# Performance work log

Measured on AMD Instinct MI355X. Metric: run time of the kernel, lower is better.

The kernel has to match this reference:

```python
import jax, jax.numpy as jnp
import numpy as np

N, D, R, E = 50000, 256, 4, 800000
LN_EPS = 1e-5
NEG_INF = -1e30  # finite stand-in for -inf so softmax stays grad-safe


def _layernorm(x, g, b):
    m = x.mean(axis=-1, keepdims=True)
    v = x.var(axis=-1, keepdims=True)
    return (x - m) / jnp.sqrt(v + LN_EPS) * g + b


def setup_inputs() -> dict:
    key = jax.random.key(0)
    ks = jax.random.split(key, 8)
    s = 1.0 / np.sqrt(D).astype(np.float32)
    return {
        'rows': jax.random.randint(ks[0], (R, E), 0, N),
        'cols': jax.random.randint(ks[1], (R, E), 0, N),
        'vals': jax.random.uniform(ks[2], (R, E), jnp.float32),
        'node_emb': jax.random.normal(ks[3], (N, D), jnp.float32) * s,
        'pre_W': jax.random.normal(ks[4], (D, D), jnp.float32) * s,
        'pre_b': jnp.zeros((D,), jnp.float32),
        'ln1_g': jnp.ones((D,), jnp.float32),
        'ln1_b': jnp.zeros((D,), jnp.float32),
        'rel_W': jax.random.normal(ks[5], (R, D, D), jnp.float32) * s,
        'attn_vec': jax.random.normal(ks[6], (D,), jnp.float32) * s,
        'self_W': jax.random.normal(ks[7], (D, D), jnp.float32) * s,
        'self_b': jnp.zeros((D,), jnp.float32),
        'bias': jnp.zeros((D,), jnp.float32),
        'ln2_g': jnp.ones((D,), jnp.float32),
        'ln2_b': jnp.zeros((D,), jnp.float32),
    }


def reference(rows, cols, vals, node_emb, pre_W, pre_b, ln1_g, ln1_b, rel_W,
              attn_vec, self_W, self_b, bias, ln2_g, ln2_b):
    # active_indices = arange(N), so x_all is the full embedding table
    x_all = node_emb
    # pre_encoder: Linear -> LayerNorm -> GELU (exact erf, torch default)
    x = jax.nn.gelu(_layernorm(x_all @ pre_W + pre_b, ln1_g, ln1_b), approximate=False)
    # per-relation: relation linear then SpMM (adj_t @ x_rel) via gather + segment_sum
    msgs = []
    for i in range(R):
        x_rel = x @ rel_W[i]                              # [N, D]
        contrib = vals[i][:, None] * x_rel[cols[i]]       # [E, D]
        msgs.append(jax.ops.segment_sum(contrib, rows[i], num_segments=N))
    stacked = jnp.stack(msgs, axis=1)                     # [N, R, D]
    # semantic attention over relations
    scores = jnp.einsum('nrd,d->nr', stacked, attn_vec)   # [N, R]
    mask = jnp.any(stacked != 0, axis=2)                  # [N, R]
    attn = jax.nn.softmax(jnp.where(mask, scores, NEG_INF), axis=1)
    attn = attn * mask                                    # == nan_to_num(softmax(-inf rows))
    out = jnp.einsum('nrd,nr->nd', stacked, attn) + bias + (x @ self_W + self_b)
    out = jax.nn.gelu(out, approximate=False)
    # active_indices = arange(N): scatter into global index space is identity
    final = _layernorm(out, ln2_g, ln2_b)
    return final, attn, x_all
```

## Files before the change

kernel.cpp:

```cpp
#include <hip/hip_runtime.h>
#include <hip/hip_fp16.h>
#include <math.h>


typedef __attribute__((ext_vector_type(8))) short bf16x8;
typedef __attribute__((ext_vector_type(4))) float f32x4;
typedef __attribute__((ext_vector_type(4))) unsigned u32x4;
typedef unsigned long long u64;

__device__ __forceinline__ float gelu_exact(float v) {
    return 0.5f * v * (1.0f + erff(v * 0.70710678118654752f));
}
__device__ __forceinline__ unsigned short f2bf(float f) {
    unsigned u = __float_as_uint(f);
    return (unsigned short)((u + 0x7fffu + ((u >> 16) & 1u)) >> 16);
}
__device__ __forceinline__ unsigned pack2(float a, float b) {
    return (unsigned)f2bf(a) | ((unsigned)f2bf(b) << 16);
}
__device__ __forceinline__ unsigned short f2h(float f) {
    return __half_as_ushort(__float2half(f));
}
__device__ __forceinline__ __half2 u2h2(unsigned u) {
    union { unsigned u; __half2 h; } c; c.u = u; return c.h;
}
__device__ __forceinline__ void gload16(const void* g, void* l) {
    __builtin_amdgcn_global_load_lds(
        (const __attribute__((address_space(1))) void*)g,
        (__attribute__((address_space(3))) void*)l, 16, 0, 0);
}

__global__ __launch_bounds__(256)
void conv_emb(const float* __restrict__ ne, unsigned short* __restrict__ emb,
              float* __restrict__ outX, int total4)
{
    const int stride = gridDim.x * blockDim.x;
    for (int i = blockIdx.x * blockDim.x + threadIdx.x; i < total4; i += stride) {
        const float4 v = reinterpret_cast<const float4*>(ne)[i];
        reinterpret_cast<float4*>(outX)[i] = v;
        ushort4 h;
        h.x = f2bf(v.x); h.y = f2bf(v.y); h.z = f2bf(v.z); h.w = f2bf(v.w);
        reinterpret_cast<ushort4*>(emb)[i] = h;
    }
}

__global__ __launch_bounds__(256)
void build_bt(const float* __restrict__ relW, const float* __restrict__ selfW,
              const float* __restrict__ preW, unsigned short* __restrict__ BTm,
              unsigned short* __restrict__ BTp)
{
    const int idx = blockIdx.x * 256 + threadIdx.x;
    if (idx < 1280 * 256) {
        const int k = idx >> 8, n = idx & 255;
        const float v = (k < 1024)
            ? relW[(size_t)(k >> 8) * 65536 + (size_t)(k & 255) * 256 + n]
            : selfW[(size_t)(k - 1024) * 256 + n];
        BTm[(size_t)n * 1280 + k] = f2bf(v);
    } else {
        const int i2 = idx - 1280 * 256;
        if (i2 < 256 * 256) {
            const int k = i2 >> 8, n = i2 & 255;
            BTp[(size_t)n * 256 + k] = f2bf(preW[(size_t)k * 256 + n]);
        }
    }
}

template<int MODE>
__global__ __launch_bounds__(512)
void gemm_mfma(const unsigned short* __restrict__ a0,
               const unsigned short* __restrict__ a1,
               const unsigned short* __restrict__ a2,
               const unsigned short* __restrict__ a3,
               const unsigned short* __restrict__ a4,
               const unsigned short* __restrict__ BT,
               const float* __restrict__ bias0, const float* __restrict__ bias1,
               const float* __restrict__ lng, const float* __restrict__ lnb,
               float* __restrict__ Cout, unsigned short* __restrict__ XOut,
               unsigned short* __restrict__ XH, int M)
{
    constexpr int K    = MODE ? 1280 : 256;
    constexpr int NSEG = MODE ? 5 : 1;

    __shared__ __align__(16) unsigned char smA[128 * 128];
    __shared__ __align__(16) unsigned char smB[256 * 128];
    __shared__ float redS[4][128];
    __shared__ float redQ[4][128];

    const int tid = threadIdx.x;
    const int w   = tid >> 6;
    const int l   = tid & 63;
    const int wm  = w >> 2, wn = w & 3;
    const int brow = blockIdx.x * 128;

    const int srow = l >> 3;
    const int sgA  = (l & 7) ^ srow;

    f32x4 acc[4][4];
#pragma unroll
    for (int mb = 0; mb < 4; ++mb)
#pragma unroll
        for (int nb = 0; nb < 4; ++nb)
            acc[mb][nb] = f32x4{0.f, 0.f, 0.f, 0.f};

    for (int seg = 0; seg < NSEG; ++seg) {
        const unsigned short* Abase =
            (MODE == 0) ? a0
                        : (seg == 0 ? a0 : seg == 1 ? a1 : seg == 2 ? a2
                                         : seg == 3 ? a3 : a4);
#pragma unroll
        for (int kk = 0; kk < 4; ++kk) {
            __syncthreads();
#pragma unroll
            for (int c = 0; c < 2; ++c) {
                const int r0 = (w * 2 + c) * 8;
                int gm = brow + r0 + srow;
                gm = min(gm, M - 1);
                gload16(Abase + ((size_t)gm << 8) + kk * 64 + sgA * 8,
                        smA + (w * 2 + c) * 1024);
            }
#pragma unroll
            for (int c = 0; c < 4; ++c) {
                const int bn = (w * 4 + c) * 8 + srow;
                gload16(BT + (size_t)bn * K + (seg * 4 + kk) * 64 + sgA * 8,
                        smB + (w * 4 + c) * 1024);
            }
            __syncthreads();

#pragma unroll
            for (int ks = 0; ks < 2; ++ks) {
                bf16x8 af[4], bf[4];
#pragma unroll
                for (int mb = 0; mb < 4; ++mb) {
                    const int row = wm * 64 + mb * 16 + (l & 15);
                    const int g   = (ks * 4 + (l >> 4)) ^ (row & 7);
                    af[mb] = *reinterpret_cast<const bf16x8*>(smA + row * 128 + g * 16);
                }
#pragma unroll
                for (int nb = 0; nb < 4; ++nb) {
                    const int row = wn * 64 + nb * 16 + (l & 15);
                    const int g   = (ks * 4 + (l >> 4)) ^ (row & 7);
                    bf[nb] = *reinterpret_cast<const bf16x8*>(smB + row * 128 + g * 16);
                }
#pragma unroll
                for (int mb = 0; mb < 4; ++mb)
#pragma unroll
                    for (int nb = 0; nb < 4; ++nb)
                        acc[mb][nb] = __builtin_amdgcn_mfma_f32_16x16x32_bf16(
                            af[mb], bf[nb], acc[mb][nb], 0, 0, 0);
            }
        }
    }

    float bb[4], gw[4], bw[4];
#pragma unroll
    for (int nb = 0; nb < 4; ++nb) {
        const int n = wn * 64 + nb * 16 + (l & 15);
        bb[nb] = bias0[n] + (MODE == 1 ? bias1[n] : 0.0f);
        gw[nb] = lng[n];
        bw[nb] = lnb[n];
    }
#pragma unroll
    for (int mb = 0; mb < 4; ++mb)
#pragma unroll
        for (int nb = 0; nb < 4; ++nb)
#pragma unroll
            for (int rg = 0; rg < 4; ++rg) {
                float v = acc[mb][nb][rg] + bb[nb];
                if (MODE == 1) v = gelu_exact(v);
                acc[mb][nb][rg] = v;
            }
#pragma unroll
    for (int mb = 0; mb < 4; ++mb)
#pragma unroll
        for (int rg = 0; rg < 4; ++rg) {
            float s = 0.f, q = 0.f;
#pragma unroll
            for (int nb = 0; nb < 4; ++nb) {
                const float v = acc[mb][nb][rg];
                s += v; q += v * v;
            }
#pragma unroll
            for (int off = 1; off < 16; off <<= 1) {
                s += __shfl_xor(s, off, 64);
                q += __shfl_xor(q, off, 64);
            }
            if ((l & 15) == 0) {
                const int row = wm * 64 + mb * 16 + (l >> 4) * 4 + rg;
                redS[wn][row] = s;
                redQ[wn][row] = q;
            }
        }
    __syncthreads();
    if (tid < 128) {
        const float s = redS[0][tid] + redS[1][tid] + redS[2][tid] + redS[3][tid];
        const float q = redQ[0][tid] + redQ[1][tid] + redQ[2][tid] + redQ[3][tid];
        const float mean = s * (1.0f / 256.0f);
        const float var  = q * (1.0f / 256.0f) - mean * mean;
        redS[0][tid] = mean;
        redQ[0][tid] = rsqrtf(var + 1e-5f);
    }
    __syncthreads();
#pragma unroll
    for (int mb = 0; mb < 4; ++mb)
#pragma unroll
        for (int rg = 0; rg < 4; ++rg) {
            const int row = wm * 64 + mb * 16 + (l >> 4) * 4 + rg;
            if (brow + row >= M) continue;
            const float mu = redS[0][row];
            const float rs = redQ[0][row];
#pragma unroll
            for (int nb = 0; nb < 4; ++nb) {
                const int n = wn * 64 + nb * 16 + (l & 15);
                const float v = (acc[mb][nb][rg] - mu) * rs * gw[nb] + bw[nb];
                if (MODE == 0) {
                    const float gv = gelu_exact(v);
                    XOut[((size_t)(brow + row) << 8) + n] = f2bf(gv);
                    XH[((size_t)(brow + row) << 8) + n]   = f2h(gv);
                } else {
                    Cout[((size_t)(brow + row) << 8) + n] = v;
                }
            }
        }
}

__global__ __launch_bounds__(256)
void wtilde_kernel(const float* __restrict__ relW, const float* __restrict__ av,
                   float* __restrict__ wt)
{
    __shared__ float avs[256];
    const int r = blockIdx.x, tid = threadIdx.x;
    avs[tid] = av[tid];
    __syncthreads();
    const float* W = relW + (size_t)r * 65536 + (size_t)tid * 256;
    float s = 0.f;
    for (int j = 0; j < 256; j += 4) {
        const float4 w4 = *reinterpret_cast<const float4*>(W + j);
        s += w4.x * avs[j] + w4.y * avs[j + 1] + w4.z * avs[j + 2] + w4.w * avs[j + 3];
    }
    wt[r * 256 + tid] = s;
}

__global__ __launch_bounds__(256)
void y_kernel(const unsigned short* __restrict__ XB, const float* __restrict__ wt,
              float* __restrict__ y, int Nn)
{
    const int n = blockIdx.x * 4 + (threadIdx.x >> 6);
    if (n >= Nn) return;
    const int l = threadIdx.x & 63;
    const uint2 d = *reinterpret_cast<const uint2*>(XB + ((size_t)n << 8) + l * 4);
    float xv[4];
    xv[0] = __uint_as_float(d.x << 16);
    xv[1] = __uint_as_float(d.x & 0xffff0000u);
    xv[2] = __uint_as_float(d.y << 16);
    xv[3] = __uint_as_float(d.y & 0xffff0000u);
    float s[4];
#pragma unroll
    for (int r = 0; r < 4; ++r) {
        const float4 w4 = *reinterpret_cast<const float4*>(wt + r * 256 + l * 4);
        s[r] = xv[0] * w4.x + xv[1] * w4.y + xv[2] * w4.z + xv[3] * w4.w;
#pragma unroll
        for (int off = 32; off; off >>= 1) s[r] += __shfl_xor(s[r], off, 64);
    }
    if (l == 0)
        *reinterpret_cast<float4*>(y + (size_t)n * 4) = make_float4(s[0], s[1], s[2], s[3]);
}

__global__ __launch_bounds__(256)
void hist_bin(const int* __restrict__ rows, int* __restrict__ cnt_t,
              int RE, int E, int Nn, int chunk, int NBIN)
{
    __shared__ int lh[800];
    const int blk = blockIdx.x;
    for (int i = threadIdx.x; i < NBIN; i += 256) lh[i] = 0;
    __syncthreads();
    const int e0 = blk * chunk;
    const int e1 = min(e0 + chunk, RE);
    for (int e = e0 + threadIdx.x; e < e1; e += 256) {
        const int r   = e / E;
        const int wid = r * Nn + rows[e];
        atomicAdd(&lh[wid >> 8], 1);
    }
    __syncthreads();
    for (int i = threadIdx.x; i < NBIN; i += 256)
        cnt_t[i * gridDim.x + blk] = lh[i];
}

__global__ __launch_bounds__(256)
void scan_blocks(const int* __restrict__ counts, int* __restrict__ offs,
                 int* __restrict__ bsums, int n)
{
    __shared__ int sh[256];
    const int t = threadIdx.x;
    const int base = blockIdx.x * 1024 + t * 4;
    int v[4], s = 0;
#pragma unroll
    for (int j = 0; j < 4; ++j) {
        v[j] = (base + j < n) ? counts[base + j] : 0;
        s += v[j];
    }
    sh[t] = s;
    __syncthreads();
    for (int off = 1; off < 256; off <<= 1) {
        const int x = (t >= off) ? sh[t - off] : 0;
        __syncthreads();
        sh[t] += x;
        __syncthreads();
    }
    int run = sh[t] - s;
    if (t == 255) bsums[blockIdx.x] = sh[255];
#pragma unroll
    for (int j = 0; j < 4; ++j) {
        if (base + j < n) offs[base + j] = run;
        run += v[j];
    }
}

__global__ __launch_bounds__(256)
void scan_bsums(int* __restrict__ bsums, int nblk)
{
    __shared__ int sh[256];
    const int t = threadIdx.x;
    const int v = (t < nblk) ? bsums[t] : 0;
    sh[t] = v;
    __syncthreads();
    for (int off = 1; off < 256; off <<= 1) {
        const int x = (t >= off) ? sh[t - off] : 0;
        __syncthreads();
        sh[t] += x;
        __syncthreads();
    }
    if (t < nblk) bsums[t] = sh[t] - v;
}

__global__ __launch_bounds__(256)
void scan_add(int* __restrict__ offs, const int* __restrict__ bsums, int n)
{
    const int i = blockIdx.x * 256 + threadIdx.x;
    if (i >= n) return;
    offs[i] += bsums[i >> 10];
}

__global__ __launch_bounds__(256)
void scatter_coarse(const int* __restrict__ rows, const int* __restrict__ cols,
                    const float* __restrict__ vals, const int* __restrict__ ctoffs,
                    u64* __restrict__ edc, int RE, int E, int Nn,
                    int chunk, int NBIN)
{
    __shared__ int lcur[800];
    const int blk = blockIdx.x;
    for (int i = threadIdx.x; i < NBIN; i += 256)
        lcur[i] = ctoffs[i * gridDim.x + blk];
    __syncthreads();
    const int e0 = blk * chunk;
    const int e1 = min(e0 + chunk, RE);
    for (int e = e0 + threadIdx.x; e < e1; e += 256) {
        const int r   = e / E;
        const int row = rows[e];
        const int wid = r * Nn + row;
        const int pos = atomicAdd(&lcur[wid >> 8], 1);
        const unsigned vb = __float_as_uint(vals[e]);
        edc[pos] = ((u64)((vb & 0xFFFFFFFCu) | (unsigned)r) << 32)
                 | ((unsigned)row << 16) | (unsigned)cols[e];
    }
}

__global__ __launch_bounds__(256)
void scatter_fine(const u64* __restrict__ edc, const int* __restrict__ ctoffs,
                  int* __restrict__ offs, u64* __restrict__ edata,
                  const float* __restrict__ y, float* __restrict__ SC,
                  int RE, int Nn, int NB1, int NBIN)
{
    __shared__ int   cnt[256];
    __shared__ int   cur[256];
    __shared__ float scr[256];
    const int bin     = blockIdx.x;
    const int widbase = bin << 8;
    const int RN      = Nn << 2;
    const int t       = threadIdx.x;
    cnt[t] = 0;
    scr[t] = 0.f;
    __syncthreads();
    const int cs = ctoffs[bin * NB1];
    const int ce = (bin + 1 < NBIN) ? ctoffs[(bin + 1) * NB1] : RE;
    for (int j = cs + t; j < ce; j += 256) {
        const u64 p = edc[j];
        const unsigned hi = (unsigned)(p >> 32);
        const unsigned lo = (unsigned)p;
        const int w = (int)(hi & 3u) * Nn + (int)(lo >> 16);
        atomicAdd(&cnt[w - widbase], 1);
    }
    __syncthreads();
    const int v = cnt[t];
    cur[t] = v;
    __syncthreads();
    for (int off = 1; off < 256; off <<= 1) {
        const int x = (t >= off) ? cur[t - off] : 0;
        __syncthreads();
        cur[t] += x;
        __syncthreads();
    }
    const int excl = cur[t] - v;
    const int wid  = widbase + t;
    if (wid < RN) offs[wid] = cs + excl;
    __syncthreads();
    cur[t] = cs + excl;
    __syncthreads();
    for (int j = cs + t; j < ce; j += 256) {
        const u64 p  = edc[j];
        const unsigned hi = (unsigned)(p >> 32);
        const unsigned lo = (unsigned)p;
        const int r   = (int)(hi & 3u);
        const int col = (int)(lo & 0xFFFFu);
        const int w   = r * Nn + (int)(lo >> 16);
        const int pos = atomicAdd(&cur[w - widbase], 1);
        edata[pos] = ((u64)(hi & 0xFFFFFFFCu) << 32) | (unsigned)col;
        const float val = __uint_as_float(hi & 0xFFFFFFFCu);
        atomicAdd(&scr[w - widbase], val * y[(size_t)col * 4 + r]);
    }
    __syncthreads();
    if (wid < RN) {
        const int r = wid / Nn;
        const int n = wid - r * Nn;
        SC[(size_t)n * 4 + r] = (v > 0) ? scr[t] : -1e30f;
    }
}

__global__ __launch_bounds__(256)
void softmax4(const float* __restrict__ scores, float* __restrict__ attn, int Nn)
{
    const int n = blockIdx.x * 256 + threadIdx.x;
    if (n >= Nn) return;
    const float4 s4 = *reinterpret_cast<const float4*>(scores + (size_t)n * 4);
    float s[4] = { s4.x, s4.y, s4.z, s4.w };
    float mx = -3.0e38f;
#pragma unroll
    for (int r = 0; r < 4; ++r) mx = fmaxf(mx, s[r]);
    float ex[4], es = 0.f;
#pragma unroll
    for (int r = 0; r < 4; ++r) { ex[r] = expf(s[r] - mx); es += ex[r]; }
    const float inv = 1.0f / es;
    float4 o;
    o.x = (s[0] > -1e29f) ? ex[0] * inv : 0.0f;
    o.y = (s[1] > -1e29f) ? ex[1] * inv : 0.0f;
    o.z = (s[2] > -1e29f) ? ex[2] * inv : 0.0f;
    o.w = (s[3] > -1e29f) ? ex[3] * inv : 0.0f;
    *reinterpret_cast<float4*>(attn + (size_t)n * 4) = o;
}

__global__ __launch_bounds__(256)
void agg_csr(const int* __restrict__ offs, const u64* __restrict__ edata,
             const unsigned short* __restrict__ xh, const float* __restrict__ attn,
             unsigned short* __restrict__ agg, int Nn, int RE)
{
    const int wid  = (blockIdx.x << 2) + (threadIdx.x >> 6);
    const int lane = threadIdx.x & 63;
    const int half = lane >> 5;
    const int sub  = lane & 31;
    const int RN   = Nn << 2;
    if (wid >= RN) return;
    const int r = wid / Nn;
    const int n = wid - r * Nn;

    const int start = offs[wid];
    const int end   = (wid + 1 < RN) ? offs[wid + 1] : RE;

    __half2 acc0 = __float2half2_rn(0.f), acc1 = acc0, acc2 = acc0, acc3 = acc0;

    int j = start + half;
    for (; j + 6 < end; j += 8) {
        u64 e[4];
#pragma unroll
        for (int q = 0; q < 4; ++q)
            e[q] = __builtin_nontemporal_load(edata + j + 2 * q);
        uint4 d[4];
        __half2 vv[4];
#pragma unroll
        for (int q = 0; q < 4; ++q) {
            const int c = (int)(e[q] & 0xffffffffu);
            vv[q] = __float2half2_rn(__uint_as_float((unsigned)(e[q] >> 32)));
            d[q]  = *reinterpret_cast<const uint4*>(xh + ((size_t)c << 8) + sub * 8);
        }
#pragma unroll
        for (int q = 0; q < 4; ++q) {
            acc0 = __hfma2(vv[q], u2h2(d[q].x), acc0);
            acc1 = __hfma2(vv[q], u2h2(d[q].y), acc1);
            acc2 = __hfma2(vv[q], u2h2(d[q].z), acc2);
            acc3 = __hfma2(vv[q], u2h2(d[q].w), acc3);
        }
    }
    for (; j < end; j += 2) {
        const u64 e0 = __builtin_nontemporal_load(edata + j);
        const int c0 = (int)(e0 & 0xffffffffu);
        const __half2 v0 = __float2half2_rn(__uint_as_float((unsigned)(e0 >> 32)));
        const uint4 d0 = *reinterpret_cast<const uint4*>(xh + ((size_t)c0 << 8) + sub * 8);
        acc0 = __hfma2(v0, u2h2(d0.x), acc0);
        acc1 = __hfma2(v0, u2h2(d0.y), acc1);
        acc2 = __hfma2(v0, u2h2(d0.z), acc2);
        acc3 = __hfma2(v0, u2h2(d0.w), acc3);
    }

    float a[8];
    a[0] = __low2float(acc0); a[1] = __high2float(acc0);
    a[2] = __low2float(acc1); a[3] = __high2float(acc1);
    a[4] = __low2float(acc2); a[5] = __high2float(acc2);
    a[6] = __low2float(acc3); a[7] = __high2float(acc3);
#pragma unroll
    for (int i = 0; i < 8; ++i) a[i] += __shfl_xor(a[i], 32, 64);

    if (half == 0) {
        const float sc = attn[(size_t)n * 4 + r];
        u32x4 st;
        st.x = pack2(sc * a[0], sc * a[1]);
        st.y = pack2(sc * a[2], sc * a[3]);
        st.z = pack2(sc * a[4], sc * a[5]);
        st.w = pack2(sc * a[6], sc * a[7]);
        __builtin_nontemporal_store(
            st, reinterpret_cast<u32x4*>(agg + ((size_t)wid << 8) + sub * 8));
    }
}

extern "C" void kernel_launch(void* const* d_in, const int* in_sizes, int n_in,
                              void* d_out, int out_size, void* d_ws, size_t ws_size,
                              hipStream_t stream)
{
    const int*   rows     = (const int*)d_in[0];
    const int*   cols     = (const int*)d_in[1];
    const float* vals     = (const float*)d_in[2];
    const float* node_emb = (const float*)d_in[3];
    const float* pre_W    = (const float*)d_in[4];
    const float* pre_b    = (const float*)d_in[5];
    const float* ln1_g    = (const float*)d_in[6];
    const float* ln1_b    = (const float*)d_in[7];
    const float* rel_W    = (const float*)d_in[8];
    const float* attn_vec = (const float*)d_in[9];
    const float* self_W   = (const float*)d_in[10];
    const float* self_b   = (const float*)d_in[11];
    const float* bias     = (const float*)d_in[12];
    const float* ln2_g    = (const float*)d_in[13];
    const float* ln2_b    = (const float*)d_in[14];

    const int Dd = 256;
    const int R  = in_sizes[8] / (Dd * Dd);
    const int N  = in_sizes[3] / Dd;
    const int E  = in_sizes[0] / R;
    const int RE = R * E;
    const int RN = R * N;

    const int NB1   = 256;
    const int chunk = (RE + NB1 - 1) / NB1;
    const int NBIN  = (RN + 255) / 256;
    const int NCT   = NBIN * NB1;

    float* out  = (float*)d_out;
    float* outF = out;
    float* outA = out + (size_t)N * Dd;
    float* outX = outA + (size_t)N * R;

    char* wp = (char*)d_ws;
    auto alloc = [&](size_t bytes) {
        char* p = wp;
        wp += (bytes + 255) & ~(size_t)255;
        return p;
    };
    unsigned short* AGGS = (unsigned short*)alloc((size_t)RN * Dd * 2);
    unsigned short* XB   = (unsigned short*)alloc((size_t)N * Dd * 2);
    unsigned short* XH   = (unsigned short*)alloc((size_t)N * Dd * 2);
    unsigned short* EMB  = (unsigned short*)alloc((size_t)N * Dd * 2);
    unsigned short* BTm  = (unsigned short*)alloc((size_t)Dd * 1280 * 2);
    unsigned short* BTp  = (unsigned short*)alloc((size_t)Dd * Dd * 2);
    float* WT   = (float*)alloc((size_t)R * Dd * 4);
    float* Y    = (float*)alloc((size_t)N * R * 4);
    float* SC   = (float*)alloc((size_t)N * R * 4);
    int* offs   = (int*)alloc((size_t)RN * 4);
    int* cnt_t  = (int*)alloc((size_t)NCT * 4);
    int* ctoffs = cnt_t;
    int* bsums2 = (int*)alloc(1024);
    u64* edata  = (u64*)alloc((size_t)RE * 8);
    u64* edc    = (u64*)alloc((size_t)RE * 8);

    const int gblocks = (N + 127) / 128;
    const int nblkC   = (NCT + 1023) / 1024;

    build_bt<<<(1280 * 256 + 256 * 256 + 255) / 256, 256, 0, stream>>>(
        rel_W, self_W, pre_W, BTm, BTp);
    conv_emb<<<2048, 256, 0, stream>>>(node_emb, EMB, outX, N * Dd / 4);

    gemm_mfma<0><<<gblocks, 512, 0, stream>>>(EMB, nullptr, nullptr, nullptr, nullptr,
                                              BTp, pre_b, nullptr, ln1_g, ln1_b,
                                              nullptr, XB, XH, N);
    wtilde_kernel<<<R, 256, 0, stream>>>(rel_W, attn_vec, WT);
    y_kernel<<<(N + 3) / 4, 256, 0, stream>>>(XB, WT, Y, N);

    hist_bin<<<NB1, 256, 0, stream>>>(rows, cnt_t, RE, E, N, chunk, NBIN);
    scan_blocks<<<nblkC, 256, 0, stream>>>(cnt_t, ctoffs, bsums2, NCT);
    scan_bsums<<<1, 256, 0, stream>>>(bsums2, nblkC);
    scan_add<<<(NCT + 255) / 256, 256, 0, stream>>>(ctoffs, bsums2, NCT);
    scatter_coarse<<<NB1, 256, 0, stream>>>(rows, cols, vals, ctoffs, edc,
                                            RE, E, N, chunk, NBIN);
    scatter_fine<<<NBIN, 256, 0, stream>>>(edc, ctoffs, offs, edata, Y, SC,
                                           RE, N, NB1, NBIN);

    softmax4<<<(N + 255) / 256, 256, 0, stream>>>(SC, outA, N);

    agg_csr<<<(RN + 3) / 4, 256, 0, stream>>>(offs, edata, XH, outA, AGGS, N, RE);

    gemm_mfma<1><<<gblocks, 512, 0, stream>>>(AGGS, AGGS + (size_t)N * Dd,
                                              AGGS + (size_t)2 * N * Dd,
                                              AGGS + (size_t)3 * N * Dd, XB,
                                              BTm, bias, self_b, ln2_g, ln2_b,
                                              outF, nullptr, nullptr, N);
}
```

Measured before the change: 560.0 us.

## Fuse attention-score projection into pre-GEMM epilogue and pack edges into 32 bits

Merges the wtilde computation into the weight-prep kernel and folds the y projection (gelu output dotted with the per-relation score vectors) into the first GEMM's epilogue, reducing through shuffles and shared memory. This removes two launches and a full re-read of XB. Edge records shrink from 64 to 32 bits: a 16-bit column plus an fp16 value. That halves edge traffic in the aggregation, but it only works if column indices fit in 16 bits, and N=50000 does. The edge value also loses precision by being rounded to fp16 earlier.

```diff
diff --git a/kernel.cpp b/kernel.cpp
--- a/kernel.cpp
+++ b/kernel.cpp
@@ -45,23 +45,37 @@
 }
 
 __global__ __launch_bounds__(256)
-void build_bt(const float* __restrict__ relW, const float* __restrict__ selfW,
-              const float* __restrict__ preW, unsigned short* __restrict__ BTm,
-              unsigned short* __restrict__ BTp)
-{
-    const int idx = blockIdx.x * 256 + threadIdx.x;
-    if (idx < 1280 * 256) {
-        const int k = idx >> 8, n = idx & 255;
-        const float v = (k < 1024)
-            ? relW[(size_t)(k >> 8) * 65536 + (size_t)(k & 255) * 256 + n]
-            : selfW[(size_t)(k - 1024) * 256 + n];
-        BTm[(size_t)n * 1280 + k] = f2bf(v);
-    } else {
-        const int i2 = idx - 1280 * 256;
-        if (i2 < 256 * 256) {
+void prep_kernel(const float* __restrict__ relW, const float* __restrict__ selfW,
+                 const float* __restrict__ preW, const float* __restrict__ av,
+                 unsigned short* __restrict__ BTm, unsigned short* __restrict__ BTp,
+                 float* __restrict__ wt)
+{
+    const int blk = blockIdx.x;
+    if (blk < 1536) {
+        const int idx = blk * 256 + threadIdx.x;
+        if (idx < 1280 * 256) {
+            const int k = idx >> 8, n = idx & 255;
+            const float v = (k < 1024)
+                ? relW[(size_t)(k >> 8) * 65536 + (size_t)(k & 255) * 256 + n]
+                : selfW[(size_t)(k - 1024) * 256 + n];
+            BTm[(size_t)n * 1280 + k] = f2bf(v);
+        } else {
+            const int i2 = idx - 1280 * 256;
             const int k = i2 >> 8, n = i2 & 255;
             BTp[(size_t)n * 256 + k] = f2bf(preW[(size_t)k * 256 + n]);
         }
+    } else {
+        __shared__ float avs[256];
+        const int r = blk - 1536, tid = threadIdx.x;
+        avs[tid] = av[tid];
+        __syncthreads();
+        const float* W = relW + (size_t)r * 65536 + (size_t)tid * 256;
+        float s = 0.f;
+        for (int j = 0; j < 256; j += 4) {
+            const float4 w4 = *reinterpret_cast<const float4*>(W + j);
+            s += w4.x * avs[j] + w4.y * avs[j + 1] + w4.z * avs[j + 2] + w4.w * avs[j + 3];
+        }
+        wt[r * 256 + tid] = s;
     }
 }
 
@@ -75,6 +89,7 @@
                const unsigned short* __restrict__ BT,
                const float* __restrict__ bias0, const float* __restrict__ bias1,
                const float* __restrict__ lng, const float* __restrict__ lnb,
+               const float* __restrict__ wt, float* __restrict__ Yout,
                float* __restrict__ Cout, unsigned short* __restrict__ XOut,
                unsigned short* __restrict__ XH, int M)
 {
@@ -200,69 +215,60 @@
         redQ[0][tid] = rsqrtf(var + 1e-5f);
     }
     __syncthreads();
+
+    float4* yred = reinterpret_cast<float4*>(smA);
+
 #pragma unroll
     for (int mb = 0; mb < 4; ++mb)
 #pragma unroll
         for (int rg = 0; rg < 4; ++rg) {
             const int row = wm * 64 + mb * 16 + (l >> 4) * 4 + rg;
-            if (brow + row >= M) continue;
             const float mu = redS[0][row];
             const float rs = redQ[0][row];
+            const bool rowok = (brow + row < M);
+            float yp0 = 0.f, yp1 = 0.f, yp2 = 0.f, yp3 = 0.f;
 #pragma unroll
             for (int nb = 0; nb < 4; ++nb) {
                 const int n = wn * 64 + nb * 16 + (l & 15);
                 const float v = (acc[mb][nb][rg] - mu) * rs * gw[nb] + bw[nb];
                 if (MODE == 0) {
                     const float gv = gelu_exact(v);
-                    XOut[((size_t)(brow + row) << 8) + n] = f2bf(gv);
-                    XH[((size_t)(brow + row) << 8) + n]   = f2h(gv);
+                    if (rowok) {
+                        XOut[((size_t)(brow + row) << 8) + n] = f2bf(gv);
+                        XH[((size_t)(brow + row) << 8) + n]   = f2h(gv);
+                    }
+                    yp0 += gv * wt[n];
+                    yp1 += gv * wt[256 + n];
+                    yp2 += gv * wt[512 + n];
+                    yp3 += gv * wt[768 + n];
                 } else {
-                    Cout[((size_t)(brow + row) << 8) + n] = v;
+                    if (rowok) Cout[((size_t)(brow + row) << 8) + n] = v;
                 }
             }
-        }
-}
-
-__global__ __launch_bounds__(256)
-void wtilde_kernel(const float* __restrict__ relW, const float* __restrict__ av,
-                   float* __restrict__ wt)
-{
-    __shared__ float avs[256];
-    const int r = blockIdx.x, tid = threadIdx.x;
-    avs[tid] = av[tid];
-    __syncthreads();
-    const float* W = relW + (size_t)r * 65536 + (size_t)tid * 256;
-    float s = 0.f;
-    for (int j = 0; j < 256; j += 4) {
-        const float4 w4 = *reinterpret_cast<const float4*>(W + j);
-        s += w4.x * avs[j] + w4.y * avs[j + 1] + w4.z * avs[j + 2] + w4.w * avs[j + 3];
-    }
-    wt[r * 256 + tid] = s;
-}
-
-__global__ __launch_bounds__(256)
-void y_kernel(const unsigned short* __restrict__ XB, const float* __restrict__ wt,
-              float* __restrict__ y, int Nn)
-{
-    const int n = blockIdx.x * 4 + (threadIdx.x >> 6);
-    if (n >= Nn) return;
-    const int l = threadIdx.x & 63;
-    const uint2 d = *reinterpret_cast<const uint2*>(XB + ((size_t)n << 8) + l * 4);
-    float xv[4];
-    xv[0] = __uint_as_float(d.x << 16);
-    xv[1] = __uint_as_float(d.x & 0xffff0000u);
-    xv[2] = __uint_as_float(d.y << 16);
-    xv[3] = __uint_as_float(d.y & 0xffff0000u);
-    float s[4];
-#pragma unroll
-    for (int r = 0; r < 4; ++r) {
-        const float4 w4 = *reinterpret_cast<const float4*>(wt + r * 256 + l * 4);
-        s[r] = xv[0] * w4.x + xv[1] * w4.y + xv[2] * w4.z + xv[3] * w4.w;
-#pragma unroll
-        for (int off = 32; off; off >>= 1) s[r] += __shfl_xor(s[r], off, 64);
-    }
-    if (l == 0)
-        *reinterpret_cast<float4*>(y + (size_t)n * 4) = make_float4(s[0], s[1], s[2], s[3]);
+            if (MODE == 0) {
+#pragma unroll
+                for (int off = 1; off < 16; off <<= 1) {
+                    yp0 += __shfl_xor(yp0, off, 64);
+                    yp1 += __shfl_xor(yp1, off, 64);
+                    yp2 += __shfl_xor(yp2, off, 64);
+                    yp3 += __shfl_xor(yp3, off, 64);
+                }
+                if ((l & 15) == 0)
+                    yred[wn * 128 + row] = make_float4(yp0, yp1, yp2, yp3);
+            }
+        }
+    if (MODE == 0) {
+        __syncthreads();
+        if (tid < 128 && brow + tid < M) {
+            const float4 a = yred[tid];
+            const float4 b = yred[128 + tid];
+            const float4 c = yred[256 + tid];
+            const float4 d = yred[384 + tid];
+            *reinterpret_cast<float4*>(Yout + (size_t)(brow + tid) * 4) =
+                make_float4(a.x + b.x + c.x + d.x, a.y + b.y + c.y + d.y,
+                            a.z + b.z + c.z + d.z, a.w + b.w + c.w + d.w);
+        }
+    }
 }
 
 __global__ __launch_bounds__(256)
@@ -366,7 +372,7 @@
 
 __global__ __launch_bounds__(256)
 void scatter_fine(const u64* __restrict__ edc, const int* __restrict__ ctoffs,
-                  int* __restrict__ offs, u64* __restrict__ edata,
+                  int* __restrict__ offs, unsigned* __restrict__ edata,
                   const float* __restrict__ y, float* __restrict__ SC,
                   int RE, int Nn, int NB1, int NBIN)
 {
@@ -413,8 +419,8 @@
         const int col = (int)(lo & 0xFFFFu);
         const int w   = r * Nn + (int)(lo >> 16);
         const int pos = atomicAdd(&cur[w - widbase], 1);
-        edata[pos] = ((u64)(hi & 0xFFFFFFFCu) << 32) | (unsigned)col;
         const float val = __uint_as_float(hi & 0xFFFFFFFCu);
+        edata[pos] = ((unsigned)f2h(val) << 16) | (unsigned)col;
         atomicAdd(&scr[w - widbase], val * y[(size_t)col * 4 + r]);
     }
     __syncthreads();
@@ -448,7 +454,7 @@
 }
 
 __global__ __launch_bounds__(256)
-void agg_csr(const int* __restrict__ offs, const u64* __restrict__ edata,
+void agg_csr(const int* __restrict__ offs, const unsigned* __restrict__ edata,
              const unsigned short* __restrict__ xh, const float* __restrict__ attn,
              unsigned short* __restrict__ agg, int Nn, int RE)
 {
@@ -468,7 +474,7 @@
 
     int j = start + half;
     for (; j + 6 < end; j += 8) {
-        u64 e[4];
+        unsigned e[4];
 #pragma unroll
         for (int q = 0; q < 4; ++q)
             e[q] = __builtin_nontemporal_load(edata + j + 2 * q);
@@ -476,8 +482,9 @@
         __half2 vv[4];
 #pragma unroll
         for (int q = 0; q < 4; ++q) {
-            const int c = (int)(e[q] & 0xffffffffu);
-            vv[q] = __float2half2_rn(__uint_as_float((unsigned)(e[q] >> 32)));
+            const int c = (int)(e[q] & 0xFFFFu);
+            const __half hv = __ushort_as_half((unsigned short)(e[q] >> 16));
+            vv[q] = __half2half2(hv);
             d[q]  = *reinterpret_cast<const uint4*>(xh + ((size_t)c << 8) + sub * 8);
         }
 #pragma unroll
@@ -489,9 +496,10 @@
         }
     }
     for (; j < end; j += 2) {
-        const u64 e0 = __builtin_nontemporal_load(edata + j);
-        const int c0 = (int)(e0 & 0xffffffffu);
-        const __half2 v0 = __float2half2_rn(__uint_as_float((unsigned)(e0 >> 32)));
+        const unsigned e0 = __builtin_nontemporal_load(edata + j);
+        const int c0 = (int)(e0 & 0xFFFFu);
+        const __half hv = __ushort_as_half((unsigned short)(e0 >> 16));
+        const __half2 v0 = __half2half2(hv);
         const uint4 d0 = *reinterpret_cast<const uint4*>(xh + ((size_t)c0 << 8) + sub * 8);
         acc0 = __hfma2(v0, u2h2(d0.x), acc0);
         acc1 = __hfma2(v0, u2h2(d0.y), acc1);
@@ -575,21 +583,19 @@
     int* cnt_t  = (int*)alloc((size_t)NCT * 4);
     int* ctoffs = cnt_t;
     int* bsums2 = (int*)alloc(1024);
-    u64* edata  = (u64*)alloc((size_t)RE * 8);
+    unsigned* edata = (unsigned*)alloc((size_t)RE * 4);
     u64* edc    = (u64*)alloc((size_t)RE * 8);
 
     const int gblocks = (N + 127) / 128;
     const int nblkC   = (NCT + 1023) / 1024;
 
-    build_bt<<<(1280 * 256 + 256 * 256 + 255) / 256, 256, 0, stream>>>(
-        rel_W, self_W, pre_W, BTm, BTp);
+    prep_kernel<<<1540, 256, 0, stream>>>(rel_W, self_W, pre_W, attn_vec,
+                                          BTm, BTp, WT);
     conv_emb<<<2048, 256, 0, stream>>>(node_emb, EMB, outX, N * Dd / 4);
 
     gemm_mfma<0><<<gblocks, 512, 0, stream>>>(EMB, nullptr, nullptr, nullptr, nullptr,
                                               BTp, pre_b, nullptr, ln1_g, ln1_b,
-                                              nullptr, XB, XH, N);
-    wtilde_kernel<<<R, 256, 0, stream>>>(rel_W, attn_vec, WT);
-    y_kernel<<<(N + 3) / 4, 256, 0, stream>>>(XB, WT, Y, N);
+                                              WT, Y, nullptr, XB, XH, N);
 
     hist_bin<<<NB1, 256, 0, stream>>>(rows, cnt_t, RE, E, N, chunk, NBIN);
     scan_blocks<<<nblkC, 256, 0, stream>>>(cnt_t, ctoffs, bsums2, NCT);
@@ -608,5 +614,6 @@
                                               AGGS + (size_t)2 * N * Dd,
                                               AGGS + (size_t)3 * N * Dd, XB,
                                               BTm, bias, self_b, ln2_g, ln2_b,
+                                              nullptr, nullptr,
                                               outF, nullptr, nullptr, N);
 }
```

New measurement: 539.4 us, median of 2. 3.7% less time.
